# Performance work log

Hardware: AMD Instinct MI355X
Metric: run time of the kernel (lower is better)

## Reference

```python
import jax, jax.numpy as jnp
import numpy as np
from jax import lax

ALPHA = 1.0
BETA = 0.001
GAMMA = 0.1
THRESHOLD = 0.5
LOG_CLAMP = -100.0  # torch BCELoss clamps log terms at -100


def setup_inputs() -> dict:
    key = jax.random.key(0)
    k1, k2 = jax.random.split(key)
    B, C, H, W = 256, 2, 192, 256
    inputs = jax.random.uniform(k1, (B, C, H, W), dtype=jnp.float32,
                                minval=1e-4, maxval=1.0 - 1e-4)
    targets = jax.random.uniform(k2, (1, B, C, H, W), dtype=jnp.float32)
    return {"inputs": inputs, "targets": targets}


def _bce(p, t):
    # mean-reduced BCE with torch-style log clamping
    logp = jnp.maximum(jnp.log(p), LOG_CLAMP)
    log1mp = jnp.maximum(jnp.log1p(-p), LOG_CLAMP)
    return -jnp.mean(t * logp + (1.0 - t) * log1mp)


def _dense_penalty(mask):
    # mask: [B, H, W] bool. Faithful to the Python loop:
    # for each column, for consecutive True rows (p, c) with p, c in [0, H-2],
    # add 1/(c-p)^3, except when p == 0 (i_before==0 is falsy in the original).
    B, H, W = mask.shape
    prev0 = jnp.zeros((B, W), dtype=jnp.int32)  # 0 encodes "no previous" (matches bug)

    def step(carry, i):
        prev, acc = carry
        m = mask[:, i, :]  # [B, W]
        dist = (i - prev).astype(jnp.float32)
        add = jnp.where(m & (prev != 0), 1.0 / (dist ** 3), 0.0)
        prev = jnp.where(m, i, prev)
        return (prev, acc + jnp.sum(add)), None

    (_, dense), _ = lax.scan(step, (prev0, jnp.float32(0.0)),
                             jnp.arange(H - 1, dtype=jnp.int32))
    return dense


def reference(inputs, targets):
    t = jnp.squeeze(targets, axis=0)  # [B, 2, H, W]
    loss_bce = ALPHA * _bce(inputs, t)
    # limit_num_cuts: count of channel-0 entries above threshold
    loss_cuts = BETA * jnp.sum(inputs[:, 0] > THRESHOLD).astype(jnp.float32)
    # avoid_dense_predictions on channel 1
    loss_dense = GAMMA * _dense_penalty(inputs[:, 1] > THRESHOLD)
    return loss_bce + loss_cuts + loss_dense
```

## Files before the change

### kernel.cpp

```cpp
#include <hip/hip_runtime.h>
#include <math.h>

#define ALPHA     1.0f
#define BETA      0.001f
#define GAMMA     0.1f
#define THRESH    0.5f
#define LOG_CLAMP -100.0f
#define LN2       0.69314718055994530942f

constexpr int B = 256, C = 2, H = 192, W = 256;
constexpr int HW   = H * W;
constexpr int HW4  = HW / 4;
constexpr long long NTOT = (long long)B * C * H * W;
constexpr int N4   = (int)(NTOT / 4);

constexpr int BCE_BLOCKS   = 2048;
constexpr int PAIRS        = 12;
constexpr int BATCH        = 6;
constexpr int DENSE_BLOCKS = 1024;
constexpr int FUSED_GRID   = DENSE_BLOCKS + BCE_BLOCKS;

typedef float vfloat4 __attribute__((ext_vector_type(4)));

__device__ __forceinline__ float fast_log(float x) {
    return fmaxf(__builtin_amdgcn_logf(x) * LN2, LOG_CLAMP);
}

__device__ __forceinline__ vfloat4 nt_load4(const vfloat4* p) {
    return __builtin_nontemporal_load(p);
}

__device__ __forceinline__ float wave_reduce(float v) {
#pragma unroll
    for (int off = 32; off > 0; off >>= 1)
        v += __shfl_down(v, off, 64);
    return v;
}

__global__ __launch_bounds__(256, 8) void fused_kernel(
        const vfloat4* __restrict__ p4,
        const vfloat4* __restrict__ t4,
        const float*   __restrict__ in,
        float2* __restrict__ part_bce,
        float*  __restrict__ part_dense) {

    if (blockIdx.x < DENSE_BLOCKS) {
        const int lane = threadIdx.x & 63;
        const int seg  = threadIdx.x >> 6;
        const int j    = blockIdx.x * 64 + lane;
        const int b    = j >> 8;
        const int w    = j & 255;
        const float* col = in + ((b * 2 + 1) * H) * W + w;
        const int segbase = seg * 48;

        int   first = -1, last = -1;
        float sum = 0.0f;
#pragma unroll
        for (int kc = 0; kc < 48; kc += 12) {
            float v[12];
#pragma unroll
            for (int k = 0; k < 12; ++k)
                v[k] = col[(segbase + kc + k) * W];
#pragma unroll
            for (int k = 0; k < 12; ++k) {
                const int i = segbase + kc + k;
                const bool m = (v[k] > THRESH) && (i != 0) && (i != 191);
                if (m) {
                    if (last >= 0) {
                        const float d = (float)(i - last);
                        sum += __builtin_amdgcn_rcpf(d * d * d);
                    } else {
                        first = i;
                    }
                    last = i;
                }
            }
        }

        __shared__ int   sfirst[256];
        __shared__ int   slast[256];
        __shared__ float ssum[256];
        sfirst[threadIdx.x] = first;
        slast[threadIdx.x]  = last;
        ssum[threadIdx.x]   = sum;
        __syncthreads();

        if (threadIdx.x < 64) {
            int   mlast = -1;
            float msum  = 0.0f;
#pragma unroll
            for (int s = 0; s < 4; ++s) {
                const int idx = s * 64 + threadIdx.x;
                const int f = sfirst[idx];
                if (f >= 0) {
                    if (mlast >= 0) {
                        const float d = (float)(f - mlast);
                        msum += __builtin_amdgcn_rcpf(d * d * d);
                    }
                    msum += ssum[idx];
                    mlast = slast[idx];
                }
            }
            float r = wave_reduce(msum);
            if (threadIdx.x == 0)
                part_dense[blockIdx.x] = r;
        }
    } else {
        const int bid  = blockIdx.x - DENSE_BLOCKS;
        const int base = bid * (256 * PAIRS) + threadIdx.x;

        float bce  = 0.0f;
        float cuts = 0.0f;

#pragma unroll
        for (int kb = 0; kb < PAIRS; kb += BATCH) {
            vfloat4 p[BATCH], t[BATCH];
#pragma unroll
            for (int u = 0; u < BATCH; ++u) {
                p[u] = nt_load4(&p4[base + (kb + u) * 256]);
                t[u] = nt_load4(&t4[base + (kb + u) * 256]);
            }
#pragma unroll
            for (int u = 0; u < BATCH; ++u) {
                const int f = base + (kb + u) * 256;
                const int c = (f / HW4) & 1;
#pragma unroll
                for (int e = 0; e < 4; ++e) {
                    const float pv = p[u][e];
                    const float tv = t[u][e];
                    const float lp = fast_log(pv);
                    const float lm = fast_log(1.0f - pv);
                    bce += lm + tv * (lp - lm);
                    if (c == 0)
                        cuts += (pv > THRESH ? 1.0f : 0.0f);
                }
            }
        }

        __shared__ float sb[4], sc[4];
        float rb = wave_reduce(bce);
        float rc = wave_reduce(cuts);
        const int lane = threadIdx.x & 63;
        const int wid  = threadIdx.x >> 6;
        if (lane == 0) { sb[wid] = rb; sc[wid] = rc; }
        __syncthreads();
        if (threadIdx.x == 0) {
            part_bce[bid] = make_float2(sb[0] + sb[1] + sb[2] + sb[3],
                                        sc[0] + sc[1] + sc[2] + sc[3]);
        }
    }
}

__global__ __launch_bounds__(256) void finalize_kernel(
        const float2* __restrict__ part_bce,
        const float* __restrict__ part_dense,
        float* __restrict__ out) {
    float b = 0.0f, c = 0.0f, d = 0.0f;
    for (int i = threadIdx.x; i < BCE_BLOCKS; i += 256) {
        float2 v = part_bce[i];
        b += v.x;
        c += v.y;
    }
    for (int i = threadIdx.x; i < DENSE_BLOCKS; i += 256)
        d += part_dense[i];

    __shared__ float sb[4], sc[4], sd[4];
    float rb = wave_reduce(b);
    float rc = wave_reduce(c);
    float rd = wave_reduce(d);
    const int lane = threadIdx.x & 63;
    const int wid  = threadIdx.x >> 6;
    if (lane == 0) { sb[wid] = rb; sc[wid] = rc; sd[wid] = rd; }
    __syncthreads();
    if (threadIdx.x == 0) {
        const float bce_sum   = sb[0] + sb[1] + sb[2] + sb[3];
        const float cuts_sum  = sc[0] + sc[1] + sc[2] + sc[3];
        const float dense_sum = sd[0] + sd[1] + sd[2] + sd[3];
        const float bce = -bce_sum / (float)NTOT;
        out[0] = ALPHA * bce + BETA * cuts_sum + GAMMA * dense_sum;
    }
}

extern "C" void kernel_launch(void* const* d_in, const int* in_sizes, int n_in,
                              void* d_out, int out_size, void* d_ws, size_t ws_size,
                              hipStream_t stream) {
    const float* inputs  = (const float*)d_in[0];
    const float* targets = (const float*)d_in[1];
    float* out = (float*)d_out;

    float2* part_bce   = (float2*)d_ws;
    float*  part_dense = (float*)d_ws + 2 * BCE_BLOCKS;

    fused_kernel<<<FUSED_GRID, 256, 0, stream>>>(
        (const vfloat4*)inputs, (const vfloat4*)targets, inputs,
        part_bce, part_dense);

    finalize_kernel<<<1, 256, 0, stream>>>(part_bce, part_dense, out);
}
```

Baseline: 206.3 us.

## Fold finalize into fused kernel via last-block atomic counter; drop log clamp

```diff
diff --git a/kernel.cpp b/kernel.cpp
--- a/kernel.cpp
+++ b/kernel.cpp
@@ -5,7 +5,6 @@
 #define BETA      0.001f
 #define GAMMA     0.1f
 #define THRESH    0.5f
-#define LOG_CLAMP -100.0f
 #define LN2       0.69314718055994530942f
 
 constexpr int B = 256, C = 2, H = 192, W = 256;
@@ -20,10 +19,15 @@
 constexpr int DENSE_BLOCKS = 1024;
 constexpr int FUSED_GRID   = DENSE_BLOCKS + BCE_BLOCKS;
 
+constexpr int WS_PBX = 0;
+constexpr int WS_PBY = 2048;
+constexpr int WS_PD  = 4096;
+constexpr int WS_CNT = 5120;
+
 typedef float vfloat4 __attribute__((ext_vector_type(4)));
 
 __device__ __forceinline__ float fast_log(float x) {
-    return fmaxf(__builtin_amdgcn_logf(x) * LN2, LOG_CLAMP);
+    return __builtin_amdgcn_logf(x) * LN2;
 }
 
 __device__ __forceinline__ vfloat4 nt_load4(const vfloat4* p) {
@@ -41,8 +45,13 @@
         const vfloat4* __restrict__ p4,
         const vfloat4* __restrict__ t4,
         const float*   __restrict__ in,
-        float2* __restrict__ part_bce,
-        float*  __restrict__ part_dense) {
+        float*  __restrict__ ws,
+        float*  __restrict__ out) {
+
+    float* pbx = ws + WS_PBX;
+    float* pby = ws + WS_PBY;
+    float* pd  = ws + WS_PD;
+    unsigned* cnt = (unsigned*)(ws + WS_CNT);
 
     if (blockIdx.x < DENSE_BLOCKS) {
         const int lane = threadIdx.x & 63;
@@ -103,7 +112,8 @@
             }
             float r = wave_reduce(msum);
             if (threadIdx.x == 0)
-                part_dense[blockIdx.x] = r;
+                __hip_atomic_store(&pd[blockIdx.x], r,
+                                   __ATOMIC_RELAXED, __HIP_MEMORY_SCOPE_AGENT);
         }
     } else {
         const int bid  = blockIdx.x - DENSE_BLOCKS;
@@ -145,37 +155,46 @@
         if (lane == 0) { sb[wid] = rb; sc[wid] = rc; }
         __syncthreads();
         if (threadIdx.x == 0) {
-            part_bce[bid] = make_float2(sb[0] + sb[1] + sb[2] + sb[3],
-                                        sc[0] + sc[1] + sc[2] + sc[3]);
-        }
-    }
-}
-
-__global__ __launch_bounds__(256) void finalize_kernel(
-        const float2* __restrict__ part_bce,
-        const float* __restrict__ part_dense,
-        float* __restrict__ out) {
-    float b = 0.0f, c = 0.0f, d = 0.0f;
+            __hip_atomic_store(&pbx[bid], sb[0] + sb[1] + sb[2] + sb[3],
+                               __ATOMIC_RELAXED, __HIP_MEMORY_SCOPE_AGENT);
+            __hip_atomic_store(&pby[bid], sc[0] + sc[1] + sc[2] + sc[3],
+                               __ATOMIC_RELAXED, __HIP_MEMORY_SCOPE_AGENT);
+        }
+    }
+
+    __shared__ bool lastflag;
+    __syncthreads();
+    if (threadIdx.x == 0) {
+        unsigned old = __hip_atomic_fetch_add(cnt, 1u,
+                           __ATOMIC_ACQ_REL, __HIP_MEMORY_SCOPE_AGENT);
+        lastflag = (old == (unsigned)(FUSED_GRID - 1));
+    }
+    __syncthreads();
+    if (!lastflag) return;
+
+    float bsum = 0.0f, csum = 0.0f, dsum = 0.0f;
     for (int i = threadIdx.x; i < BCE_BLOCKS; i += 256) {
-        float2 v = part_bce[i];
-        b += v.x;
-        c += v.y;
+        bsum += __hip_atomic_load(&pbx[i], __ATOMIC_RELAXED,
+                                  __HIP_MEMORY_SCOPE_AGENT);
+        csum += __hip_atomic_load(&pby[i], __ATOMIC_RELAXED,
+                                  __HIP_MEMORY_SCOPE_AGENT);
     }
     for (int i = threadIdx.x; i < DENSE_BLOCKS; i += 256)
-        d += part_dense[i];
-
-    __shared__ float sb[4], sc[4], sd[4];
-    float rb = wave_reduce(b);
-    float rc = wave_reduce(c);
-    float rd = wave_reduce(d);
+        dsum += __hip_atomic_load(&pd[i], __ATOMIC_RELAXED,
+                                  __HIP_MEMORY_SCOPE_AGENT);
+
+    __shared__ float fb[4], fc[4], fd[4];
+    float rb = wave_reduce(bsum);
+    float rc = wave_reduce(csum);
+    float rd = wave_reduce(dsum);
     const int lane = threadIdx.x & 63;
     const int wid  = threadIdx.x >> 6;
-    if (lane == 0) { sb[wid] = rb; sc[wid] = rc; sd[wid] = rd; }
+    if (lane == 0) { fb[wid] = rb; fc[wid] = rc; fd[wid] = rd; }
     __syncthreads();
     if (threadIdx.x == 0) {
-        const float bce_sum   = sb[0] + sb[1] + sb[2] + sb[3];
-        const float cuts_sum  = sc[0] + sc[1] + sc[2] + sc[3];
-        const float dense_sum = sd[0] + sd[1] + sd[2] + sd[3];
+        const float bce_sum   = fb[0] + fb[1] + fb[2] + fb[3];
+        const float cuts_sum  = fc[0] + fc[1] + fc[2] + fc[3];
+        const float dense_sum = fd[0] + fd[1] + fd[2] + fd[3];
         const float bce = -bce_sum / (float)NTOT;
         out[0] = ALPHA * bce + BETA * cuts_sum + GAMMA * dense_sum;
     }
@@ -187,13 +206,11 @@
     const float* inputs  = (const float*)d_in[0];
     const float* targets = (const float*)d_in[1];
     float* out = (float*)d_out;
-
-    float2* part_bce   = (float2*)d_ws;
-    float*  part_dense = (float*)d_ws + 2 * BCE_BLOCKS;
+    float* ws  = (float*)d_ws;
+
+    hipMemsetAsync((char*)d_ws + WS_CNT * sizeof(float), 0, sizeof(unsigned),
+                   stream);
 
     fused_kernel<<<FUSED_GRID, 256, 0, stream>>>(
-        (const vfloat4*)inputs, (const vfloat4*)targets, inputs,
-        part_bce, part_dense);
-
-    finalize_kernel<<<1, 256, 0, stream>>>(part_bce, part_dense, out);
-}
+        (const vfloat4*)inputs, (const vfloat4*)targets, inputs, ws, out);
+}
```

New measurement: 355.8 us. +72.5%, slower.
